# Optimization experiments

Hardware: AMD Instinct MI355X
Metric: run time of the kernel (lower is better)

Reference implementation:

```python
import jax, jax.numpy as jnp
import numpy as np

S, B, D = 1024, 4, 1024
H, HK = 16, 64
FF = 4096
ROT = 32
EPS = 1e-8
THETA = 10000.0


def rmsnorm(x, scale):
    # RMSNorm with p<0: full-dim L2 norm / sqrt(d)
    norm = jnp.linalg.norm(x, axis=-1, keepdims=True)
    rms = norm * (D ** -0.5)
    return scale * (x / (rms + EPS))


def rope(x):
    # x: [b,h,s,hk]; rotate first ROT features (interleaved-pair convention
    # of rotary_embedding_torch), pass the rest through.
    s = x.shape[-2]
    inv_freq = 1.0 / (THETA ** (jnp.arange(0, ROT, 2, dtype=jnp.float32) / ROT))
    freqs = jnp.arange(s, dtype=jnp.float32)[:, None] * inv_freq  # [s, ROT/2]
    freqs = jnp.repeat(freqs, 2, axis=-1)                          # [s, ROT]
    cos, sin = jnp.cos(freqs), jnp.sin(freqs)
    r, p = x[..., :ROT], x[..., ROT:]
    x1, x2 = r[..., 0::2], r[..., 1::2]
    r_half = jnp.stack((-x2, x1), axis=-1).reshape(r.shape)
    return jnp.concatenate([r * cos + r_half * sin, p], axis=-1)


def split_heads(x):
    # [s,b,D] -> [b,H,s,HK]
    s, b, _ = x.shape
    return jnp.transpose(x, (1, 0, 2)).reshape(b, s, H, HK).transpose(0, 2, 1, 3)


def combine_heads(x):
    # [b,H,s,HK] -> [s,b,D]
    b, _, s, _ = x.shape
    return jnp.transpose(x.transpose(0, 2, 1, 3).reshape(b, s, D), (1, 0, 2))


def mha(q_in, k_in, v_in, wq, bq, wk, bk, wv, bv, wo, bo, mask):
    Q = rope(split_heads(q_in @ wq + bq))
    K = rope(split_heads(k_in @ wk + bk))
    V = split_heads(v_in @ wv + bv)
    scores = jnp.einsum('bhqk,bhsk->bhqs', Q, K) / np.float32(np.sqrt(HK))
    if mask is not None:
        scores = jnp.where(mask == 0, jnp.float32(-1e9), scores)
    probs = jax.nn.softmax(scores, axis=-1)
    out = jnp.einsum('bhqs,bhsk->bhqk', probs, V)
    return combine_heads(out) @ wo + bo


def setup_inputs() -> dict:
    key = jax.random.key(0)
    ks = jax.random.split(key, 24)
    w = lambda k, shp: jax.random.normal(k, shp, jnp.float32) * 0.02
    inp = {
        'x': jax.random.normal(ks[0], (S, B, D), jnp.float32),
        'enc_output': jax.random.normal(ks[1], (S, B, D), jnp.float32),
        'tgt_mask': jnp.tril(jnp.ones((1, 1, S, S), jnp.int32)),
    }
    i = 2
    for pfx in ('sa', 'ca'):
        for nm in ('wq', 'wk', 'wv', 'wo'):
            inp[f'{pfx}_{nm}'] = w(ks[i], (D, D)); i += 1
            inp[f'{pfx}_{nm[1]}b' if False else f'{pfx}_b{nm[1]}'] = jnp.zeros((D,), jnp.float32)
    inp['ff_w1'] = w(ks[i], (D, FF)); i += 1
    inp['ff_b1'] = jnp.zeros((FF,), jnp.float32)
    inp['ff_w2'] = w(ks[i], (FF, D)); i += 1
    inp['ff_b2'] = jnp.zeros((D,), jnp.float32)
    inp['g1'] = jnp.ones((D,), jnp.float32)
    inp['g2'] = jnp.ones((D,), jnp.float32)
    inp['g3'] = jnp.ones((D,), jnp.float32)
    return inp


def reference(x, enc_output, tgt_mask,
              sa_wq, sa_bq, sa_wk, sa_bk, sa_wv, sa_bv, sa_wo, sa_bo,
              ca_wq, ca_bq, ca_wk, ca_bk, ca_wv, ca_bv, ca_wo, ca_bo,
              ff_w1, ff_b1, ff_w2, ff_b2, g1, g2, g3):
    xn = rmsnorm(x, g1)
    x = x + mha(xn, xn, xn, sa_wq, sa_bq, sa_wk, sa_bk, sa_wv, sa_bv, sa_wo, sa_bo, tgt_mask)
    xn = rmsnorm(x, g2)
    x = x + mha(xn, enc_output, enc_output, ca_wq, ca_bq, ca_wk, ca_bk, ca_wv, ca_bv, ca_wo, ca_bo, None)
    xn = rmsnorm(x, g3)
    h = jax.nn.silu(xn @ ff_w1 + ff_b1)
    x = x + (h @ ff_w2 + ff_b2)
    return x
```

## Files before the change

kernel.cpp:

```cpp
#include <hip/hip_runtime.h>
#include <hip/hip_bf16.h>
#include <math.h>

#define SS 1024
#define BB 4
#define DD 1024
#define HH 16
#define FFF 4096
#define MM (SS*BB)

typedef __attribute__((ext_vector_type(8))) short bf16x8;
typedef __attribute__((ext_vector_type(4))) float f32x4;

#define VM_WAIT(n) asm volatile("s_waitcnt vmcnt(" #n ")" ::: "memory")
#define MEM_FENCE() asm volatile("" ::: "memory")

__global__ void rmsnorm_kernel(const float* __restrict__ x, const float* __restrict__ g,
                               __hip_bfloat16* __restrict__ out) {
    int row = blockIdx.x;
    const float* xr = x + (size_t)row * DD;
    int tid = threadIdx.x;
    float4 v = *reinterpret_cast<const float4*>(xr + tid * 4);
    float ss = v.x*v.x + v.y*v.y + v.z*v.z + v.w*v.w;
    #pragma unroll
    for (int off = 32; off; off >>= 1) ss += __shfl_down(ss, off);
    __shared__ float part[4];
    if ((tid & 63) == 0) part[tid >> 6] = ss;
    __syncthreads();
    float tot = part[0] + part[1] + part[2] + part[3];
    float rms = sqrtf(tot) * (1.0f / 32.0f);
    float inv = 1.0f / (rms + 1e-8f);
    float4 gv = *reinterpret_cast<const float4*>(g + tid * 4);
    union { __hip_bfloat16 h[4]; uint2 u; } p;
    p.h[0] = __float2bfloat16(gv.x * v.x * inv);
    p.h[1] = __float2bfloat16(gv.y * v.y * inv);
    p.h[2] = __float2bfloat16(gv.z * v.z * inv);
    p.h[3] = __float2bfloat16(gv.w * v.w * inv);
    reinterpret_cast<uint2*>(out + (size_t)row * DD)[tid] = p.u;
}

__global__ void f2b_kernel(const float* __restrict__ in, __hip_bfloat16* __restrict__ out) {
    int i = blockIdx.x * 256 + threadIdx.x;
    float4 v = reinterpret_cast<const float4*>(in)[i];
    union { __hip_bfloat16 h[4]; uint2 u; } p;
    p.h[0] = __float2bfloat16(v.x);
    p.h[1] = __float2bfloat16(v.y);
    p.h[2] = __float2bfloat16(v.z);
    p.h[3] = __float2bfloat16(v.w);
    reinterpret_cast<uint2*>(out)[i] = p.u;
}

__global__ void addf_kernel(float* __restrict__ out, const float* __restrict__ p) {
    int i = blockIdx.x * 256 + threadIdx.x;
    float4 a = reinterpret_cast<const float4*>(out)[i];
    float4 b = reinterpret_cast<const float4*>(p)[i];
    a.x += b.x; a.y += b.y; a.z += b.z; a.w += b.w;
    reinterpret_cast<float4*>(out)[i] = a;
}

__global__ void bias_concat(const float* __restrict__ a, const float* __restrict__ b,
                            const float* __restrict__ c, float* __restrict__ o, int n) {
    int total = (c ? 3 : 2) * n;
    int i = blockIdx.x * 256 + threadIdx.x;
    if (i >= total) return;
    int seg = i / n, off = i - seg * n;
    const float* p = seg == 0 ? a : (seg == 1 ? b : c);
    o[i] = p[off];
}

__global__ void wtrans8_kernel(const float* s0, const float* s1, const float* s2, const float* s3,
                               const float* s4, const float* s5, const float* s6, const float* s7,
                               __hip_bfloat16* d0, __hip_bfloat16* d1, __hip_bfloat16* d2,
                               __hip_bfloat16* d3, __hip_bfloat16* d4, __hip_bfloat16* d5,
                               __hip_bfloat16* d6, __hip_bfloat16* d7) {
    const float* W; __hip_bfloat16* Wt;
    switch (blockIdx.z) {
        case 0: W = s0; Wt = d0; break;
        case 1: W = s1; Wt = d1; break;
        case 2: W = s2; Wt = d2; break;
        case 3: W = s3; Wt = d3; break;
        case 4: W = s4; Wt = d4; break;
        case 5: W = s5; Wt = d5; break;
        case 6: W = s6; Wt = d6; break;
        default: W = s7; Wt = d7; break;
    }
    __shared__ float tile[32][33];
    int n0 = blockIdx.x * 32, k0 = blockIdx.y * 32;
    int tx = threadIdx.x & 31, ty = threadIdx.x >> 5;
    #pragma unroll
    for (int i = 0; i < 4; i++) {
        int kk = ty + i * 8;
        tile[kk][tx] = W[(size_t)(k0 + kk) * DD + n0 + tx];
    }
    __syncthreads();
    #pragma unroll
    for (int i = 0; i < 4; i++) {
        int nn = ty + i * 8;
        Wt[(size_t)(n0 + nn) * DD + k0 + tx] = __float2bfloat16(tile[tx][nn]);
    }
}

__global__ void wtrans_kernel(const float* __restrict__ W, __hip_bfloat16* __restrict__ Wt,
                              int K, int N) {
    __shared__ float tile[32][33];
    int n0 = blockIdx.x * 32, k0 = blockIdx.y * 32;
    int tx = threadIdx.x & 31, ty = threadIdx.x >> 5;
    #pragma unroll
    for (int i = 0; i < 4; i++) {
        int kk = ty + i * 8;
        tile[kk][tx] = W[(size_t)(k0 + kk) * N + n0 + tx];
    }
    __syncthreads();
    #pragma unroll
    for (int i = 0; i < 4; i++) {
        int nn = ty + i * 8;
        Wt[(size_t)(n0 + nn) * K + k0 + tx] = __float2bfloat16(tile[tx][nn]);
    }
}

template<int EPI, int BM, int BN>
__global__ __launch_bounds__(256) void gemm_bf16(
    const __hip_bfloat16* __restrict__ A, const __hip_bfloat16* __restrict__ Bt,
    const float* __restrict__ bias, const float* __restrict__ res,
    float* __restrict__ Cf, __hip_bfloat16* __restrict__ Cb, int K, int N)
{
    constexpr int MFRAG = BM / 32;
    constexpr int NFRAG = BN / 32;
    constexpr int WM = BM / 2, WN = BN / 2;
    constexpr int LPT = (BM + BN) / 32;
    __shared__ __hip_bfloat16 As[2][BM * 64];
    __shared__ __hip_bfloat16 Bs[2][BN * 64];
    int tid = threadIdx.x;
    int lane = tid & 63, w = tid >> 6;
    int wr = w >> 1, wc = w & 1;

    int gx = gridDim.x;
    int nwg = gx * gridDim.y;
    int orig = blockIdx.y * gx + blockIdx.x;
    int qd = nwg >> 3, rr2 = nwg & 7, xcd = orig & 7, pos = orig >> 3;
    int lin = (xcd < rr2 ? xcd * (qd + 1) : rr2 * (qd + 1) + (xcd - rr2) * qd) + pos;
    int brow = (lin / gx) * BM, bcol = (lin % gx) * BN;

    f32x4 acc[MFRAG][NFRAG];
    #pragma unroll
    for (int m = 0; m < MFRAG; m++)
        #pragma unroll
        for (int n = 0; n < NFRAG; n++)
            acc[m][n] = (f32x4){0.f, 0.f, 0.f, 0.f};

    const __hip_bfloat16* Ab = A + (size_t)brow * K;
    const __hip_bfloat16* Bb = Bt + (size_t)bcol * K;

    auto stage = [&](int buf, int kt) {
        #pragma unroll
        for (int i = 0; i < BM / 32; i++) {
            int f = i * 256 + tid;
            int row = f >> 3, cp = f & 7;
            int cs = cp ^ (row & 7);
            __builtin_amdgcn_global_load_lds(
                (const __attribute__((address_space(1))) void*)(Ab + (size_t)row * K + kt + cs * 8),
                (__attribute__((address_space(3))) void*)(As[buf] + (size_t)(i * 256 + w * 64) * 8),
                16, 0, 0);
        }
        #pragma unroll
        for (int i = 0; i < BN / 32; i++) {
            int f = i * 256 + tid;
            int row = f >> 3, cp = f & 7;
            int cs = cp ^ (row & 7);
            __builtin_amdgcn_global_load_lds(
                (const __attribute__((address_space(1))) void*)(Bb + (size_t)row * K + kt + cs * 8),
                (__attribute__((address_space(3))) void*)(Bs[buf] + (size_t)(i * 256 + w * 64) * 8),
                16, 0, 0);
        }
    };

    int nt = K >> 6;
    stage(0, 0);
    if (nt > 1) stage(1, 64);

    int cb = 0;
    int r = lane & 15, g = lane >> 4;
    for (int t = 0; t < nt; t++) {
        if (t + 1 < nt) {
            if constexpr (LPT == 4) VM_WAIT(4); else VM_WAIT(8);
        } else VM_WAIT(0);
        __builtin_amdgcn_s_barrier();
        MEM_FENCE();

        bf16x8 aF[2][MFRAG], bF[2][NFRAG];
        #pragma unroll
        for (int kk = 0; kk < 2; kk++) {
            #pragma unroll
            for (int m = 0; m < MFRAG; m++) {
                int row = WM * wr + m * 16 + r;
                aF[kk][m] = *reinterpret_cast<const bf16x8*>(
                    As[cb] + (size_t)row * 64 + (size_t)((kk * 4 + g) ^ (row & 7)) * 8);
            }
            #pragma unroll
            for (int n = 0; n < NFRAG; n++) {
                int row = WN * wc + n * 16 + r;
                bF[kk][n] = *reinterpret_cast<const bf16x8*>(
                    Bs[cb] + (size_t)row * 64 + (size_t)((kk * 4 + g) ^ (row & 7)) * 8);
            }
        }
        __builtin_amdgcn_s_setprio(1);
        #pragma unroll
        for (int kk = 0; kk < 2; kk++)
            #pragma unroll
            for (int m = 0; m < MFRAG; m++)
                #pragma unroll
                for (int n = 0; n < NFRAG; n++)
                    acc[m][n] = __builtin_amdgcn_mfma_f32_16x16x32_bf16(aF[kk][m], bF[kk][n], acc[m][n], 0, 0, 0);
        __builtin_amdgcn_s_setprio(0);

        MEM_FENCE();
        __builtin_amdgcn_s_barrier();
        if (t + 2 < nt) stage(cb, (t + 2) << 6);
        cb ^= 1;
    }

    int row0 = brow + WM * wr + (g * 4);
    int col0 = bcol + WN * wc + r;
    #pragma unroll
    for (int m = 0; m < MFRAG; m++) {
        #pragma unroll
        for (int n = 0; n < NFRAG; n++) {
            int ccol = col0 + n * 16;
            float bv = bias[ccol];
            #pragma unroll
            for (int q = 0; q < 4; q++) {
                int rrow = row0 + m * 16 + q;
                float o = acc[m][n][q] + bv;
                if (EPI == 0) {
                    Cb[(size_t)rrow * N + ccol] = __float2bfloat16(o);
                } else if (EPI == 1) {
                    o = o / (1.0f + __expf(-o));
                    Cb[(size_t)rrow * N + ccol] = __float2bfloat16(o);
                } else {
                    o += res[(size_t)rrow * N + ccol];
                    Cf[(size_t)rrow * N + ccol] = o;
                }
            }
        }
    }
}

__global__ __launch_bounds__(256) void gemm_splitk(
    const __hip_bfloat16* __restrict__ A, const __hip_bfloat16* __restrict__ Bt,
    const float* __restrict__ bias, const float* __restrict__ res,
    float* __restrict__ Cf, float* __restrict__ P1, int K, int N)
{
    constexpr int BM = 64, BN = 64;
    constexpr int MFRAG = 2, NFRAG = 2;
    constexpr int WM = 32, WN = 32;
    __shared__ __hip_bfloat16 As[2][BM * 64];
    __shared__ __hip_bfloat16 Bs[2][BN * 64];
    int tid = threadIdx.x;
    int lane = tid & 63, w = tid >> 6;
    int wr = w >> 1, wc = w & 1;

    int gx = gridDim.x;
    int nwg = gx * gridDim.y;
    int orig = blockIdx.y * gx + blockIdx.x;
    int qd = nwg >> 3, rr2 = nwg & 7, xcd = orig & 7, pos = orig >> 3;
    int lin = (xcd < rr2 ? xcd * (qd + 1) : rr2 * (qd + 1) + (xcd - rr2) * qd) + pos;
    int brow = (lin / gx) * BM, bcol = (lin % gx) * BN;
    int k0 = blockIdx.z * (K >> 1);

    f32x4 acc[MFRAG][NFRAG];
    #pragma unroll
    for (int m = 0; m < MFRAG; m++)
        #pragma unroll
        for (int n = 0; n < NFRAG; n++)
            acc[m][n] = (f32x4){0.f, 0.f, 0.f, 0.f};

    const __hip_bfloat16* Ab = A + (size_t)brow * K + k0;
    const __hip_bfloat16* Bb = Bt + (size_t)bcol * K + k0;

    auto stage = [&](int buf, int kt) {
        #pragma unroll
        for (int i = 0; i < 2; i++) {
            int f = i * 256 + tid;
            int row = f >> 3, cp = f & 7;
            int cs = cp ^ (row & 7);
            __builtin_amdgcn_global_load_lds(
                (const __attribute__((address_space(1))) void*)(Ab + (size_t)row * K + kt + cs * 8),
                (__attribute__((address_space(3))) void*)(As[buf] + (size_t)(i * 256 + w * 64) * 8),
                16, 0, 0);
        }
        #pragma unroll
        for (int i = 0; i < 2; i++) {
            int f = i * 256 + tid;
            int row = f >> 3, cp = f & 7;
            int cs = cp ^ (row & 7);
            __builtin_amdgcn_global_load_lds(
                (const __attribute__((address_space(1))) void*)(Bb + (size_t)row * K + kt + cs * 8),
                (__attribute__((address_space(3))) void*)(Bs[buf] + (size_t)(i * 256 + w * 64) * 8),
                16, 0, 0);
        }
    };

    int nt = K >> 7;
    stage(0, 0);
    if (nt > 1) stage(1, 64);

    int cb = 0;
    int r = lane & 15, g = lane >> 4;
    for (int t = 0; t < nt; t++) {
        if (t + 1 < nt) VM_WAIT(4); else VM_WAIT(0);
        __builtin_amdgcn_s_barrier();
        MEM_FENCE();

        bf16x8 aF[2][MFRAG], bF[2][NFRAG];
        #pragma unroll
        for (int kk = 0; kk < 2; kk++) {
            #pragma unroll
            for (int m = 0; m < MFRAG; m++) {
                int row = WM * wr + m * 16 + r;
                aF[kk][m] = *reinterpret_cast<const bf16x8*>(
                    As[cb] + (size_t)row * 64 + (size_t)((kk * 4 + g) ^ (row & 7)) * 8);
            }
            #pragma unroll
            for (int n = 0; n < NFRAG; n++) {
                int row = WN * wc + n * 16 + r;
                bF[kk][n] = *reinterpret_cast<const bf16x8*>(
                    Bs[cb] + (size_t)row * 64 + (size_t)((kk * 4 + g) ^ (row & 7)) * 8);
            }
        }
        __builtin_amdgcn_s_setprio(1);
        #pragma unroll
        for (int kk = 0; kk < 2; kk++)
            #pragma unroll
            for (int m = 0; m < MFRAG; m++)
                #pragma unroll
                for (int n = 0; n < NFRAG; n++)
                    acc[m][n] = __builtin_amdgcn_mfma_f32_16x16x32_bf16(aF[kk][m], bF[kk][n], acc[m][n], 0, 0, 0);
        __builtin_amdgcn_s_setprio(0);

        MEM_FENCE();
        __builtin_amdgcn_s_barrier();
        if (t + 2 < nt) stage(cb, (t + 2) << 6);
        cb ^= 1;
    }

    int row0 = brow + WM * wr + (g * 4);
    int col0 = bcol + WN * wc + r;
    #pragma unroll
    for (int m = 0; m < MFRAG; m++) {
        #pragma unroll
        for (int n = 0; n < NFRAG; n++) {
            int ccol = col0 + n * 16;
            float bv = bias[ccol];
            #pragma unroll
            for (int q = 0; q < 4; q++) {
                int rrow = row0 + m * 16 + q;
                if (blockIdx.z == 0) {
                    Cf[(size_t)rrow * N + ccol] =
                        acc[m][n][q] + bv + res[(size_t)rrow * N + ccol];
                } else {
                    P1[(size_t)rrow * N + ccol] = acc[m][n][q];
                }
            }
        }
    }
}

__global__ __launch_bounds__(256) void qkv_prep(
    const __hip_bfloat16* __restrict__ Q, int qs,
    const __hip_bfloat16* __restrict__ K, int ks2,
    const __hip_bfloat16* __restrict__ V, int vs,
    __hip_bfloat16* __restrict__ Qh, __hip_bfloat16* __restrict__ Kh,
    __hip_bfloat16* __restrict__ Vt, float qscale)
{
    int tid = threadIdx.x;
    int bh = blockIdx.y;
    int b = bh >> 4, h = bh & 15;
    int s0 = blockIdx.x * 64;
    #pragma unroll
    for (int sel = 0; sel < 2; sel++) {
        const __hip_bfloat16* src = sel ? K : Q;
        int stride = sel ? ks2 : qs;
        __hip_bfloat16* dst = sel ? Kh : Qh;
        float sc = sel ? 1.0f : qscale;
        #pragma unroll
        for (int it = 0; it < 2; it++) {
            int f = it * 256 + tid;
            int i = f >> 3, c8 = f & 7;
            int s = s0 + i;
            union { uint4 u; __hip_bfloat16 hh[8]; } d;
            d.u = *reinterpret_cast<const uint4*>(src + (size_t)(s * BB + b) * stride + h * 64 + c8 * 8);
            float fv[8];
            #pragma unroll
            for (int e = 0; e < 8; e++) fv[e] = __bfloat162float(d.hh[e]);
            if (c8 < 4) {
                #pragma unroll
                for (int pp = 0; pp < 4; pp++) {
                    int p = c8 * 4 + pp;
                    float ang = (float)s * __powf(10000.f, -(float)p * (1.0f / 16.0f));
                    float cc, sn;
                    __sincosf(ang, &sn, &cc);
                    float x0 = fv[pp * 2], x1 = fv[pp * 2 + 1];
                    fv[pp * 2]     = x0 * cc - x1 * sn;
                    fv[pp * 2 + 1] = x1 * cc + x0 * sn;
                }
            }
            #pragma unroll
            for (int e = 0; e < 8; e++) d.hh[e] = __float2bfloat16(fv[e] * sc);
            *reinterpret_cast<uint4*>(dst + ((size_t)bh * SS + s) * 64 + c8 * 8) = d.u;
        }
    }
    __shared__ __hip_bfloat16 t[64][72];
    #pragma unroll
    for (int i = 0; i < 2; i++) {
        int f = tid + i * 256;
        int sr = f >> 3, c = (f & 7) * 8;
        *reinterpret_cast<uint4*>(&t[sr][c]) =
            *reinterpret_cast<const uint4*>(V + (size_t)((s0 + sr) * BB + b) * vs + h * 64 + c);
    }
    __syncthreads();
    #pragma unroll
    for (int i = 0; i < 2; i++) {
        int f = tid + i * 256;
        int d = f >> 3, c = (f & 7) * 8;
        __hip_bfloat16 tmp[8];
        #pragma unroll
        for (int j = 0; j < 8; j++) tmp[j] = t[c + j][d];
        *reinterpret_cast<uint4*>(Vt + ((size_t)bh * 64 + d) * SS + s0 + c) =
            *reinterpret_cast<uint4*>(tmp);
    }
}

template<bool CAUSAL>
__global__ __launch_bounds__(512) void attn_mfma(
    const __hip_bfloat16* __restrict__ Qh, const __hip_bfloat16* __restrict__ Kh,
    const __hip_bfloat16* __restrict__ Vth, __hip_bfloat16* __restrict__ O)
{
    __shared__ __hip_bfloat16 Ks[2][64 * 64];
    __shared__ __hip_bfloat16 Vs[2][64 * 64];
    __shared__ __hip_bfloat16 Ps[8][16][72];
    int tid = threadIdx.x, lane = tid & 63, w = tid >> 6;
    int r = lane & 15, g = lane >> 4;

    int lin = blockIdx.y * gridDim.x + blockIdx.x;
    int bh = (lin & 7) * 8 + ((lin >> 3) & 7);
    int qblk = lin >> 6;
    int b = bh >> 4, h = bh & 15;
    int qb = qblk * 128;
    const __hip_bfloat16* gQ = Qh + (size_t)bh * SS * 64;
    const __hip_bfloat16* gK = Kh + (size_t)bh * SS * 64;
    const __hip_bfloat16* gV = Vth + (size_t)bh * 64 * SS;

    bf16x8 qf0 = *reinterpret_cast<const bf16x8*>(gQ + (size_t)(qb + w * 16 + r) * 64 + g * 8);
    bf16x8 qf1 = *reinterpret_cast<const bf16x8*>(gQ + (size_t)(qb + w * 16 + r) * 64 + 32 + g * 8);

    const short oneb = (short)0x3F80;
    bf16x8 onesV = {oneb, oneb, oneb, oneb, oneb, oneb, oneb, oneb};

    f32x4 accO[4];
    f32x4 accL = (f32x4){0.f, 0.f, 0.f, 0.f};
    #pragma unroll
    for (int j = 0; j < 4; j++) accO[j] = (f32x4){0.f, 0.f, 0.f, 0.f};

    int nt = CAUSAL ? 2 * (qblk + 1) : (SS / 64);

    auto stage = [&](int buf, int kt) {
        int row = tid >> 3, cp = tid & 7;
        int cs = cp ^ (row & 7);
        __builtin_amdgcn_global_load_lds(
            (const __attribute__((address_space(1))) void*)(gK + (size_t)(kt + row) * 64 + cs * 8),
            (__attribute__((address_space(3))) void*)(&Ks[buf][(size_t)tid * 8]),
            16, 0, 0);
        __builtin_amdgcn_global_load_lds(
            (const __attribute__((address_space(1))) void*)(gV + (size_t)row * SS + kt + cs * 8),
            (__attribute__((address_space(3))) void*)(&Vs[buf][(size_t)tid * 8]),
            16, 0, 0);
    };

    stage(0, 0);
    if (nt > 1) stage(1, 64);
    int cb = 0;
    for (int t = 0; t < nt; t++) {
        if (t + 1 < nt) VM_WAIT(2); else VM_WAIT(0);
        __builtin_amdgcn_s_barrier();
        MEM_FENCE();
        int kt = t * 64;

        f32x4 sa[4];
        __builtin_amdgcn_s_setprio(1);
        #pragma unroll
        for (int ks = 0; ks < 4; ks++) {
            sa[ks] = (f32x4){0.f, 0.f, 0.f, 0.f};
            int rk = ks * 16 + r;
            bf16x8 kf0 = *reinterpret_cast<const bf16x8*>(&Ks[cb][rk * 64 + ((g ^ (rk & 7)) * 8)]);
            bf16x8 kf1 = *reinterpret_cast<const bf16x8*>(&Ks[cb][rk * 64 + (((4 + g) ^ (rk & 7)) * 8)]);
            sa[ks] = __builtin_amdgcn_mfma_f32_16x16x32_bf16(qf0, kf0, sa[ks], 0, 0, 0);
            sa[ks] = __builtin_amdgcn_mfma_f32_16x16x32_bf16(qf1, kf1, sa[ks], 0, 0, 0);
        }
        __builtin_amdgcn_s_setprio(0);

        if (CAUSAL && t >= nt - 2) {
            #pragma unroll
            for (int ks = 0; ks < 4; ks++) {
                int key = kt + ks * 16 + r;
                #pragma unroll
                for (int j = 0; j < 4; j++) {
                    int qq = qb + w * 16 + g * 4 + j;
                    if (key > qq) sa[ks][j] = -1e9f;
                }
            }
        }

        #pragma unroll
        for (int ks = 0; ks < 4; ks++)
            #pragma unroll
            for (int j = 0; j < 4; j++)
                Ps[w][g * 4 + j][ks * 16 + r] = __float2bfloat16(exp2f(sa[ks][j]));

        __builtin_amdgcn_s_setprio(1);
        #pragma unroll
        for (int ks2 = 0; ks2 < 2; ks2++) {
            bf16x8 pf = *reinterpret_cast<const bf16x8*>(&Ps[w][r][ks2 * 32 + g * 8]);
            accL = __builtin_amdgcn_mfma_f32_16x16x32_bf16(pf, onesV, accL, 0, 0, 0);
            #pragma unroll
            for (int ds = 0; ds < 4; ds++) {
                int rv = ds * 16 + r;
                bf16x8 vf = *reinterpret_cast<const bf16x8*>(
                    &Vs[cb][rv * 64 + (((ks2 * 4 + g) ^ (rv & 7)) * 8)]);
                accO[ds] = __builtin_amdgcn_mfma_f32_16x16x32_bf16(pf, vf, accO[ds], 0, 0, 0);
            }
        }
        __builtin_amdgcn_s_setprio(0);

        MEM_FENCE();
        __builtin_amdgcn_s_barrier();
        if (t + 2 < nt) stage(cb, (t + 2) * 64);
        cb ^= 1;
    }

    #pragma unroll
    for (int j = 0; j < 4; j++) {
        float inv = 1.0f / accL[j];
        int s = qb + w * 16 + g * 4 + j;
        #pragma unroll
        for (int ds = 0; ds < 4; ds++)
            O[(size_t)(s * BB + b) * DD + h * 64 + ds * 16 + r] =
                __float2bfloat16(accO[ds][j] * inv);
    }
}

extern "C" void kernel_launch(void* const* d_in, const int* in_sizes, int n_in,
                              void* d_out, int out_size, void* d_ws, size_t ws_size,
                              hipStream_t stream) {
    const float* x    = (const float*)d_in[0];
    const float* enc  = (const float*)d_in[1];
    const float* sa_wq = (const float*)d_in[3];
    const float* sa_bq = (const float*)d_in[4];
    const float* sa_wk = (const float*)d_in[5];
    const float* sa_bk = (const float*)d_in[6];
    const float* sa_wv = (const float*)d_in[7];
    const float* sa_bv = (const float*)d_in[8];
    const float* sa_wo = (const float*)d_in[9];
    const float* sa_bo = (const float*)d_in[10];
    const float* ca_wq = (const float*)d_in[11];
    const float* ca_bq = (const float*)d_in[12];
    const float* ca_wk = (const float*)d_in[13];
    const float* ca_bk = (const float*)d_in[14];
    const float* ca_wv = (const float*)d_in[15];
    const float* ca_bv = (const float*)d_in[16];
    const float* ca_wo = (const float*)d_in[17];
    const float* ca_bo = (const float*)d_in[18];
    const float* ff_w1 = (const float*)d_in[19];
    const float* ff_b1 = (const float*)d_in[20];
    const float* ff_w2 = (const float*)d_in[21];
    const float* ff_b2 = (const float*)d_in[22];
    const float* g1 = (const float*)d_in[23];
    const float* g2 = (const float*)d_in[24];
    const float* g3 = (const float*)d_in[25];
    float* out = (float*)d_out;

    const size_t MB = 1024 * 1024;
    char* base = (char*)d_ws;
    __hip_bfloat16* sa_qkvT = (__hip_bfloat16*)(base + 0 * MB);
    __hip_bfloat16* sa_woT  = (__hip_bfloat16*)(base + 6 * MB);
    __hip_bfloat16* ca_wqT  = (__hip_bfloat16*)(base + 8 * MB);
    __hip_bfloat16* ca_kvT  = (__hip_bfloat16*)(base + 10 * MB);
    __hip_bfloat16* ca_woT  = (__hip_bfloat16*)(base + 14 * MB);
    __hip_bfloat16* w1T     = (__hip_bfloat16*)(base + 16 * MB);
    __hip_bfloat16* w2T     = (__hip_bfloat16*)(base + 24 * MB);
    float* sa_bqkv = (float*)(base + 32 * MB);
    float* ca_bkv  = (float*)(base + 32 * MB + 16384);
    __hip_bfloat16* xnb   = (__hip_bfloat16*)(base + 33 * MB);
    __hip_bfloat16* qkv   = (__hip_bfloat16*)(base + 41 * MB);
    __hip_bfloat16* Qhp   = (__hip_bfloat16*)(base + 65 * MB);
    __hip_bfloat16* Khp   = (__hip_bfloat16*)(base + 73 * MB);
    __hip_bfloat16* Vtp   = (__hip_bfloat16*)(base + 81 * MB);
    float* x1 = (float*)(base + 96 * MB);
    __hip_bfloat16* attnb = xnb;
    __hip_bfloat16* encb  = Qhp;
    __hip_bfloat16* qn    = qkv;
    __hip_bfloat16* kvb   = qkv + (size_t)4 * MB;
    __hip_bfloat16* hb    = qkv;
    float* P1sk = (float*)(base + 73 * MB);

    const float QSCALE = 0.125f * 1.44269504089f;

    dim3 blk(256);
    dim3 blk512(512);
    dim3 gT8(32, 32, 8);
    dim3 gW1(FFF / 32, DD / 32);
    dim3 gW2(DD / 32, FFF / 32);
    dim3 gQKV(3072 / 128, MM / 128);
    dim3 gKV(2048 / 128, MM / 128);
    dim3 g64(DD / 64, MM / 64);
    dim3 gF1(FFF / 128, MM / 128);
    dim3 gSK(DD / 64, MM / 64, 2);
    dim3 gPrep(SS / 64, BB * HH);
    dim3 gAtt(SS / 128, BB * HH);

    wtrans8_kernel<<<gT8, blk, 0, stream>>>(
        sa_wq, sa_wk, sa_wv, sa_wo, ca_wq, ca_wk, ca_wv, ca_wo,
        sa_qkvT, sa_qkvT + (size_t)1024 * DD, sa_qkvT + (size_t)2048 * DD, sa_woT,
        ca_wqT, ca_kvT, ca_kvT + (size_t)1024 * DD, ca_woT);
    wtrans_kernel<<<gW1, blk, 0, stream>>>(ff_w1, w1T, DD, FFF);
    wtrans_kernel<<<gW2, blk, 0, stream>>>(ff_w2, w2T, FFF, DD);
    bias_concat<<<12, blk, 0, stream>>>(sa_bq, sa_bk, sa_bv, sa_bqkv, DD);
    bias_concat<<<8, blk, 0, stream>>>(ca_bk, ca_bv, nullptr, ca_bkv, DD);

    rmsnorm_kernel<<<MM, blk, 0, stream>>>(x, g1, xnb);
    gemm_bf16<0, 128, 128><<<gQKV, blk, 0, stream>>>(xnb, sa_qkvT, sa_bqkv, nullptr, nullptr, qkv, DD, 3072);
    qkv_prep<<<gPrep, blk, 0, stream>>>(qkv, 3072, qkv + 1024, 3072, qkv + 2048, 3072,
                                        Qhp, Khp, Vtp, QSCALE);
    attn_mfma<true><<<gAtt, blk512, 0, stream>>>(Qhp, Khp, Vtp, attnb);
    gemm_bf16<2, 64, 64><<<g64, blk, 0, stream>>>(attnb, sa_woT, sa_bo, x, x1, nullptr, DD, DD);

    rmsnorm_kernel<<<MM, blk, 0, stream>>>(x1, g2, xnb);
    f2b_kernel<<<(MM * DD / 4) / 256, blk, 0, stream>>>(enc, encb);
    gemm_bf16<0, 128, 128><<<gKV, blk, 0, stream>>>(encb, ca_kvT, ca_bkv, nullptr, nullptr, kvb, DD, 2048);
    gemm_bf16<0, 64, 64><<<g64, blk, 0, stream>>>(xnb, ca_wqT, ca_bq, nullptr, nullptr, qn, DD, DD);
    qkv_prep<<<gPrep, blk, 0, stream>>>(qn, 1024, kvb, 2048, kvb + 1024, 2048,
                                        Qhp, Khp, Vtp, QSCALE);
    attn_mfma<false><<<gAtt, blk512, 0, stream>>>(Qhp, Khp, Vtp, attnb);
    gemm_bf16<2, 64, 64><<<g64, blk, 0, stream>>>(attnb, ca_woT, ca_bo, x1, x1, nullptr, DD, DD);

    rmsnorm_kernel<<<MM, blk, 0, stream>>>(x1, g3, xnb);
    gemm_bf16<1, 128, 128><<<gF1, blk, 0, stream>>>(xnb, w1T, ff_b1, nullptr, nullptr, hb, DD, FFF);
    gemm_splitk<<<gSK, blk, 0, stream>>>(hb, w2T, ff_b2, x1, out, P1sk, FFF, DD);
    addf_kernel<<<(MM * DD / 4) / 256, blk, 0, stream>>>(out, P1sk);
}
```

Measured before the change: 363.2 us.

## Use 256x256 eight-wave GEMM for FFN1 and drop split-K for FFN2

Replaces the split-K FFN2 GEMM and its separate add kernel with a plain 64x64 GEMM whose epilogue adds the residual directly. The FFN1 GEMM moves to a new 512-thread kernel with 256x256 tiles, which gives more data reuse per LDS load. The FFN1 grid becomes 16x16 = 256 workgroups. The large tile needs 128KB of LDS and many accumulator registers, so occupancy drops to one block per CU. The FFN2 GEMM also loses the extra parallelism it had from splitting K.

```diff
diff --git a/kernel.cpp b/kernel.cpp
--- a/kernel.cpp
+++ b/kernel.cpp
@@ -48,14 +48,6 @@
     p.h[2] = __float2bfloat16(v.z);
     p.h[3] = __float2bfloat16(v.w);
     reinterpret_cast<uint2*>(out)[i] = p.u;
-}
-
-__global__ void addf_kernel(float* __restrict__ out, const float* __restrict__ p) {
-    int i = blockIdx.x * 256 + threadIdx.x;
-    float4 a = reinterpret_cast<const float4*>(out)[i];
-    float4 b = reinterpret_cast<const float4*>(p)[i];
-    a.x += b.x; a.y += b.y; a.z += b.z; a.w += b.w;
-    reinterpret_cast<float4*>(out)[i] = a;
 }
 
 __global__ void bias_concat(const float* __restrict__ a, const float* __restrict__ b,
@@ -245,19 +237,18 @@
     }
 }
 
-__global__ __launch_bounds__(256) void gemm_splitk(
+template<int EPI>
+__global__ __launch_bounds__(512) void gemm8w_bf16(
     const __hip_bfloat16* __restrict__ A, const __hip_bfloat16* __restrict__ Bt,
-    const float* __restrict__ bias, const float* __restrict__ res,
-    float* __restrict__ Cf, float* __restrict__ P1, int K, int N)
+    const float* __restrict__ bias, __hip_bfloat16* __restrict__ Cb, int K, int N)
 {
-    constexpr int BM = 64, BN = 64;
-    constexpr int MFRAG = 2, NFRAG = 2;
-    constexpr int WM = 32, WN = 32;
+    constexpr int BM = 256, BN = 256;
+    constexpr int MFRAG = 8, NFRAG = 4;
     __shared__ __hip_bfloat16 As[2][BM * 64];
     __shared__ __hip_bfloat16 Bs[2][BN * 64];
     int tid = threadIdx.x;
     int lane = tid & 63, w = tid >> 6;
-    int wr = w >> 1, wc = w & 1;
+    int wr = w >> 2, wc = w & 3;
 
     int gx = gridDim.x;
     int nwg = gx * gridDim.y;
@@ -265,7 +256,6 @@
     int qd = nwg >> 3, rr2 = nwg & 7, xcd = orig & 7, pos = orig >> 3;
     int lin = (xcd < rr2 ? xcd * (qd + 1) : rr2 * (qd + 1) + (xcd - rr2) * qd) + pos;
     int brow = (lin / gx) * BM, bcol = (lin % gx) * BN;
-    int k0 = blockIdx.z * (K >> 1);
 
     f32x4 acc[MFRAG][NFRAG];
     #pragma unroll
@@ -274,68 +264,66 @@
         for (int n = 0; n < NFRAG; n++)
             acc[m][n] = (f32x4){0.f, 0.f, 0.f, 0.f};
 
-    const __hip_bfloat16* Ab = A + (size_t)brow * K + k0;
-    const __hip_bfloat16* Bb = Bt + (size_t)bcol * K + k0;
+    const __hip_bfloat16* Ab = A + (size_t)brow * K;
+    const __hip_bfloat16* Bb = Bt + (size_t)bcol * K;
 
     auto stage = [&](int buf, int kt) {
         #pragma unroll
-        for (int i = 0; i < 2; i++) {
-            int f = i * 256 + tid;
+        for (int i = 0; i < 4; i++) {
+            int f = i * 512 + tid;
             int row = f >> 3, cp = f & 7;
             int cs = cp ^ (row & 7);
             __builtin_amdgcn_global_load_lds(
                 (const __attribute__((address_space(1))) void*)(Ab + (size_t)row * K + kt + cs * 8),
-                (__attribute__((address_space(3))) void*)(As[buf] + (size_t)(i * 256 + w * 64) * 8),
+                (__attribute__((address_space(3))) void*)(As[buf] + (size_t)(i * 512 + w * 64) * 8),
                 16, 0, 0);
         }
         #pragma unroll
-        for (int i = 0; i < 2; i++) {
-            int f = i * 256 + tid;
+        for (int i = 0; i < 4; i++) {
+            int f = i * 512 + tid;
             int row = f >> 3, cp = f & 7;
             int cs = cp ^ (row & 7);
             __builtin_amdgcn_global_load_lds(
                 (const __attribute__((address_space(1))) void*)(Bb + (size_t)row * K + kt + cs * 8),
-                (__attribute__((address_space(3))) void*)(Bs[buf] + (size_t)(i * 256 + w * 64) * 8),
+                (__attribute__((address_space(3))) void*)(Bs[buf] + (size_t)(i * 512 + w * 64) * 8),
                 16, 0, 0);
         }
     };
 
-    int nt = K >> 7;
+    int nt = K >> 6;
     stage(0, 0);
     if (nt > 1) stage(1, 64);
 
     int cb = 0;
     int r = lane & 15, g = lane >> 4;
     for (int t = 0; t < nt; t++) {
-        if (t + 1 < nt) VM_WAIT(4); else VM_WAIT(0);
+        if (t + 1 < nt) VM_WAIT(8); else VM_WAIT(0);
         __builtin_amdgcn_s_barrier();
         MEM_FENCE();
 
-        bf16x8 aF[2][MFRAG], bF[2][NFRAG];
         #pragma unroll
         for (int kk = 0; kk < 2; kk++) {
+            bf16x8 aF[MFRAG], bF[NFRAG];
             #pragma unroll
             for (int m = 0; m < MFRAG; m++) {
-                int row = WM * wr + m * 16 + r;
-                aF[kk][m] = *reinterpret_cast<const bf16x8*>(
+                int row = 128 * wr + m * 16 + r;
+                aF[m] = *reinterpret_cast<const bf16x8*>(
                     As[cb] + (size_t)row * 64 + (size_t)((kk * 4 + g) ^ (row & 7)) * 8);
             }
             #pragma unroll
             for (int n = 0; n < NFRAG; n++) {
-                int row = WN * wc + n * 16 + r;
-                bF[kk][n] = *reinterpret_cast<const bf16x8*>(
+                int row = 64 * wc + n * 16 + r;
+                bF[n] = *reinterpret_cast<const bf16x8*>(
                     Bs[cb] + (size_t)row * 64 + (size_t)((kk * 4 + g) ^ (row & 7)) * 8);
             }
-        }
-        __builtin_amdgcn_s_setprio(1);
-        #pragma unroll
-        for (int kk = 0; kk < 2; kk++)
+            __builtin_amdgcn_s_setprio(1);
             #pragma unroll
             for (int m = 0; m < MFRAG; m++)
                 #pragma unroll
                 for (int n = 0; n < NFRAG; n++)
-                    acc[m][n] = __builtin_amdgcn_mfma_f32_16x16x32_bf16(aF[kk][m], bF[kk][n], acc[m][n], 0, 0, 0);
-        __builtin_amdgcn_s_setprio(0);
+                    acc[m][n] = __builtin_amdgcn_mfma_f32_16x16x32_bf16(aF[m], bF[n], acc[m][n], 0, 0, 0);
+            __builtin_amdgcn_s_setprio(0);
+        }
 
         MEM_FENCE();
         __builtin_amdgcn_s_barrier();
@@ -343,8 +331,8 @@
         cb ^= 1;
     }
 
-    int row0 = brow + WM * wr + (g * 4);
-    int col0 = bcol + WN * wc + r;
+    int row0 = brow + 128 * wr + (g * 4);
+    int col0 = bcol + 64 * wc + r;
     #pragma unroll
     for (int m = 0; m < MFRAG; m++) {
         #pragma unroll
@@ -354,12 +342,9 @@
             #pragma unroll
             for (int q = 0; q < 4; q++) {
                 int rrow = row0 + m * 16 + q;
-                if (blockIdx.z == 0) {
-                    Cf[(size_t)rrow * N + ccol] =
-                        acc[m][n][q] + bv + res[(size_t)rrow * N + ccol];
-                } else {
-                    P1[(size_t)rrow * N + ccol] = acc[m][n][q];
-                }
+                float o = acc[m][n][q] + bv;
+                if (EPI == 1) o = o / (1.0f + __expf(-o));
+                Cb[(size_t)rrow * N + ccol] = __float2bfloat16(o);
             }
         }
     }
@@ -600,7 +585,6 @@
     __hip_bfloat16* qn    = qkv;
     __hip_bfloat16* kvb   = qkv + (size_t)4 * MB;
     __hip_bfloat16* hb    = qkv;
-    float* P1sk = (float*)(base + 73 * MB);
 
     const float QSCALE = 0.125f * 1.44269504089f;
 
@@ -611,9 +595,8 @@
     dim3 gW2(DD / 32, FFF / 32);
     dim3 gQKV(3072 / 128, MM / 128);
     dim3 gKV(2048 / 128, MM / 128);
+    dim3 gF1(FFF / 256, MM / 256);
     dim3 g64(DD / 64, MM / 64);
-    dim3 gF1(FFF / 128, MM / 128);
-    dim3 gSK(DD / 64, MM / 64, 2);
     dim3 gPrep(SS / 64, BB * HH);
     dim3 gAtt(SS / 128, BB * HH);
 
@@ -643,7 +626,6 @@
     gemm_bf16<2, 64, 64><<<g64, blk, 0, stream>>>(attnb, ca_woT, ca_bo, x1, x1, nullptr, DD, DD);
 
     rmsnorm_kernel<<<MM, blk, 0, stream>>>(x1, g3, xnb);
-    gemm_bf16<1, 128, 128><<<gF1, blk, 0, stream>>>(xnb, w1T, ff_b1, nullptr, nullptr, hb, DD, FFF);
-    gemm_splitk<<<gSK, blk, 0, stream>>>(hb, w2T, ff_b2, x1, out, P1sk, FFF, DD);
-    addf_kernel<<<(MM * DD / 4) / 256, blk, 0, stream>>>(out, P1sk);
-}
+    gemm8w_bf16<1><<<gF1, blk512, 0, stream>>>(xnb, w1T, ff_b1, hb, DD, FFF);
+    gemm_bf16<2, 64, 64><<<g64, blk, 0, stream>>>(hb, w2T, ff_b2, x1, out, nullptr, FFF, DD);
+}
```

Measured after the change: 346.3 us, median of 2. 4.6% less time.
